# Kernel optimization log

Measured on AMD Instinct MI355X. Metric: run time of the kernel, lower is better.

Reference implementation:

```python
import jax, jax.numpy as jnp
import numpy as np

H = 1024   # d_model
N = 64     # state size (N//2 complex modes)
L_VAL = 4096
DT_MIN, DT_MAX = 1e-3, 0.1


def setup_inputs() -> dict:
    key = jax.random.key(0)
    k1, k2 = jax.random.split(key, 2)
    log_dt = (jax.random.uniform(k1, (H,), dtype=jnp.float32)
              * (np.float32(np.log(DT_MAX)) - np.float32(np.log(DT_MIN)))
              + np.float32(np.log(DT_MIN)))
    C_real = jax.random.normal(k2, (H, N // 2, 2), dtype=jnp.float32)
    # parameterization='exp': log_A_real = log(0.5)
    log_A_real = jnp.full((H, N // 2), np.float32(np.log(0.5)), dtype=jnp.float32)
    A_imag = np.float32(np.pi) * jnp.broadcast_to(
        jnp.arange(N // 2, dtype=jnp.float32), (H, N // 2))
    return {"C_real": C_real, "log_dt": log_dt, "log_A_real": log_A_real,
            "A_imag": A_imag, "L": L_VAL}


def reference(C_real, log_dt, log_A_real, A_imag, L):
    dt = jnp.exp(log_dt)                              # (H,)
    C = C_real[..., 0] + 1j * C_real[..., 1]          # (H, N/2) complex
    A = -jnp.exp(log_A_real) + 1j * A_imag            # (H, N/2) complex ('exp' param)
    dtA = A * dt[:, None]                             # (H, N/2)
    # C <- C * (exp(dtA) - 1) / A
    Ct = C * (jnp.exp(dtA) - 1.0) / A                 # (H, N/2)
    # Vandermonde: exp(dtA[:, :, None] * arange(L)) -> (H, N/2, L)
    V = jnp.exp(dtA[:, :, None] * jnp.arange(L, dtype=jnp.float32))
    K = 2.0 * jnp.einsum('hn,hnl->hl', Ct, V).real    # (H, L) real
    return K
```

## Files before the change

### kernel.cpp

```cpp
#include <hip/hip_runtime.h>
#include <math.h>

#define NMODES 32
#define INV2PI 0.15915494309189535f

typedef short bf16x8 __attribute__((ext_vector_type(8)));
typedef float f32x4  __attribute__((ext_vector_type(4)));

__device__ inline void sincos_rev(float rev, float& s, float& c) {
    float f = rev - floorf(rev);
    s = __builtin_amdgcn_sinf(f);
    c = __builtin_amdgcn_cosf(f);
}

__device__ inline void split_bf(float x, short& hi, short& lo) {
    const unsigned u = __float_as_uint(x);
    const float xf = __uint_as_float(u & 0xFFFF0000u);
    hi = (short)(u >> 16);
    const float r = x - xf;
    lo = (short)(__float_as_uint(r) >> 16);
}

__global__ __launch_bounds__(256, 4) void ssm_mfma_kernel(
    const float* __restrict__ C_real,
    const float* __restrict__ log_dt,
    const float* __restrict__ log_A_real,
    const float* __restrict__ A_imag,
    float* __restrict__ K,
    int L)
{
    __shared__ bf16x8 ldsB[16][64];

    const int h    = blockIdx.x;
    const int tid  = threadIdx.x;
    const int w    = tid >> 6;
    const int lane = tid & 63;
    const int r    = lane & 15;
    const int g    = lane >> 4;

    const float dt = __expf(log_dt[h]);

    float dAr_[8], rhi_[8], rlo_[8], Ctr_[8], Cti_[8];

#pragma unroll
    for (int j = 0; j < 8; ++j) {
        const int m   = g * 8 + j;
        const int idx = h * NMODES + m;
        const float Ar = -__expf(log_A_real[idx]);
        const float Ai = A_imag[idx];
        const float dAr = dt * Ar;
        const float dAi_rev = dt * Ai * INV2PI;

        const float rhi = __uint_as_float(__float_as_uint(dAi_rev) & 0xFFFFF000u);
        const float rlo = dAi_rev - rhi;

        float sn, cs;
        sincos_rev(dAi_rev, sn, cs);
        const float er   = __expf(dAr);
        const float em1r = er * cs - 1.0f;
        const float em1i = er * sn;
        const float inv  = 1.0f / (Ar * Ar + Ai * Ai);
        const float fr   = (em1r * Ar + em1i * Ai) * inv;
        const float fi   = (em1i * Ar - em1r * Ai) * inv;
        const float Cr   = C_real[idx * 2 + 0];
        const float Ci   = C_real[idx * 2 + 1];
        Ctr_[j] = Cr * fr - Ci * fi;
        Cti_[j] = Cr * fi + Ci * fr;
        dAr_[j] = dAr; rhi_[j] = rhi; rlo_[j] = rlo;
    }

    {
        bf16x8 bh0, bl0, bh1, bl1;
        const float d = (float)(r + 16 * w);
#pragma unroll
        for (int j = 0; j < 8; ++j) {
            const float pm = __expf(dAr_[j] * d);
            const float p  = rhi_[j] * d;
            const float f  = (p - floorf(p)) + rlo_[j] * d;
            float qs, qc;
            sincos_rev(f, qs, qc);
            short hh, ll;
            split_bf(pm * qc, hh, ll); bh0[j] = hh; bl0[j] = ll;
            split_bf(pm * qs, hh, ll); bh1[j] = hh; bl1[j] = ll;
        }
        ldsB[w * 4 + 0][lane] = bh0;
        ldsB[w * 4 + 1][lane] = bl0;
        ldsB[w * 4 + 2][lane] = bh1;
        ldsB[w * 4 + 3][lane] = bl1;
    }

    bf16x8 Ah0, Al0, Ah1, Al1;
    {
        const float t = (float)(64 * (r + 16 * w));
#pragma unroll
        for (int j = 0; j < 8; ++j) {
            const float pm = __expf(dAr_[j] * t);
            const float p  = rhi_[j] * t;
            const float f  = (p - floorf(p)) + rlo_[j] * t;
            float zs, zc;
            sincos_rev(f, zs, zc);
            const float gr  = (Ctr_[j] * zc - Cti_[j] * zs) * pm;
            const float gni = -(Ctr_[j] * zs + Cti_[j] * zc) * pm;
            short hh, ll;
            split_bf(gr, hh, ll);  Ah0[j] = hh; Al0[j] = ll;
            split_bf(gni, hh, ll); Ah1[j] = hh; Al1[j] = ll;
        }
    }

    __syncthreads();

    float* __restrict__ Kh = K + (size_t)h * L;

#pragma unroll
    for (int b = 0; b < 4; ++b) {
        const bf16x8 Bh0 = ldsB[b * 4 + 0][lane];
        const bf16x8 Bl0 = ldsB[b * 4 + 1][lane];
        const bf16x8 Bh1 = ldsB[b * 4 + 2][lane];
        const bf16x8 Bl1 = ldsB[b * 4 + 3][lane];
        f32x4 acc = {0.f, 0.f, 0.f, 0.f};
        acc = __builtin_amdgcn_mfma_f32_16x16x32_bf16(Ah0, Bh0, acc, 0, 0, 0);
        acc = __builtin_amdgcn_mfma_f32_16x16x32_bf16(Ah1, Bh1, acc, 0, 0, 0);
        acc = __builtin_amdgcn_mfma_f32_16x16x32_bf16(Ah0, Bl0, acc, 0, 0, 0);
        acc = __builtin_amdgcn_mfma_f32_16x16x32_bf16(Ah1, Bl1, acc, 0, 0, 0);
        acc = __builtin_amdgcn_mfma_f32_16x16x32_bf16(Al0, Bh0, acc, 0, 0, 0);
        acc = __builtin_amdgcn_mfma_f32_16x16x32_bf16(Al1, Bh1, acc, 0, 0, 0);
#pragma unroll
        for (int reg = 0; reg < 4; ++reg) {
            Kh[64 * (16 * w + 4 * g + reg) + 16 * b + r] = 2.0f * acc[reg];
        }
    }
}

extern "C" void kernel_launch(void* const* d_in, const int* in_sizes, int n_in,
                              void* d_out, int out_size, void* d_ws, size_t ws_size,
                              hipStream_t stream) {
    const float* C_real     = (const float*)d_in[0];
    const float* log_dt     = (const float*)d_in[1];
    const float* log_A_real = (const float*)d_in[2];
    const float* A_imag     = (const float*)d_in[3];
    float* K = (float*)d_out;

    const int H = in_sizes[1];
    const int L = out_size / H;

    ssm_mfma_kernel<<<H, 256, 0, stream>>>(
        C_real, log_dt, log_A_real, A_imag, K, L);
}
```

Before: 14.16 us.

## Compute per-mode coefficients once via LDS and swap MFMA operands for float4 stores

```diff
diff --git a/kernel.cpp b/kernel.cpp
--- a/kernel.cpp
+++ b/kernel.cpp
@@ -29,7 +29,9 @@
     float* __restrict__ K,
     int L)
 {
-    __shared__ bf16x8 ldsB[16][64];
+    __shared__ __align__(16) float sDAr[NMODES], sRhi[NMODES], sRlo[NMODES],
+                                   sCtr[NMODES], sCti[NMODES];
+    __shared__ bf16x8 sB[16][64];
 
     const int h    = blockIdx.x;
     const int tid  = threadIdx.x;
@@ -38,14 +40,10 @@
     const int r    = lane & 15;
     const int g    = lane >> 4;
 
-    const float dt = __expf(log_dt[h]);
-
-    float dAr_[8], rhi_[8], rlo_[8], Ctr_[8], Cti_[8];
-
-#pragma unroll
-    for (int j = 0; j < 8; ++j) {
-        const int m   = g * 8 + j;
+    {
+        const int m   = tid & 31;
         const int idx = h * NMODES + m;
+        const float dt = __expf(log_dt[h]);
         const float Ar = -__expf(log_A_real[idx]);
         const float Ai = A_imag[idx];
         const float dAr = dt * Ar;
@@ -64,9 +62,40 @@
         const float fi   = (em1i * Ar - em1r * Ai) * inv;
         const float Cr   = C_real[idx * 2 + 0];
         const float Ci   = C_real[idx * 2 + 1];
-        Ctr_[j] = Cr * fr - Ci * fi;
-        Cti_[j] = Cr * fi + Ci * fr;
-        dAr_[j] = dAr; rhi_[j] = rhi; rlo_[j] = rlo;
+        if (tid < 32) {
+            sDAr[m] = dAr; sRhi[m] = rhi; sRlo[m] = rlo;
+            sCtr[m] = Cr * fr - Ci * fi;
+            sCti[m] = Cr * fi + Ci * fr;
+        }
+    }
+    __syncthreads();
+
+    float dAr_[8], rhi_[8], rlo_[8];
+#pragma unroll
+    for (int j = 0; j < 8; ++j) {
+        dAr_[j] = sDAr[g * 8 + j];
+        rhi_[j] = sRhi[g * 8 + j];
+        rlo_[j] = sRlo[g * 8 + j];
+    }
+
+    bf16x8 Ah0, Al0, Ah1, Al1;
+    {
+        const float t = (float)(64 * (r + 16 * w));
+#pragma unroll
+        for (int j = 0; j < 8; ++j) {
+            const float Ctr = sCtr[g * 8 + j];
+            const float Cti = sCti[g * 8 + j];
+            const float pm = __expf(dAr_[j] * t);
+            const float p  = rhi_[j] * t;
+            const float f  = (p - floorf(p)) + rlo_[j] * t;
+            float zs, zc;
+            sincos_rev(f, zs, zc);
+            const float gr  = (Ctr * zc - Cti * zs) * pm;
+            const float gni = -(Ctr * zs + Cti * zc) * pm;
+            short hh, ll;
+            split_bf(gr, hh, ll);  Ah0[j] = hh; Al0[j] = ll;
+            split_bf(gni, hh, ll); Ah1[j] = hh; Al1[j] = ll;
+        }
     }
 
     {
@@ -83,51 +112,32 @@
             split_bf(pm * qc, hh, ll); bh0[j] = hh; bl0[j] = ll;
             split_bf(pm * qs, hh, ll); bh1[j] = hh; bl1[j] = ll;
         }
-        ldsB[w * 4 + 0][lane] = bh0;
-        ldsB[w * 4 + 1][lane] = bl0;
-        ldsB[w * 4 + 2][lane] = bh1;
-        ldsB[w * 4 + 3][lane] = bl1;
+        sB[w * 4 + 0][lane] = bh0;
+        sB[w * 4 + 1][lane] = bl0;
+        sB[w * 4 + 2][lane] = bh1;
+        sB[w * 4 + 3][lane] = bl1;
     }
-
-    bf16x8 Ah0, Al0, Ah1, Al1;
-    {
-        const float t = (float)(64 * (r + 16 * w));
-#pragma unroll
-        for (int j = 0; j < 8; ++j) {
-            const float pm = __expf(dAr_[j] * t);
-            const float p  = rhi_[j] * t;
-            const float f  = (p - floorf(p)) + rlo_[j] * t;
-            float zs, zc;
-            sincos_rev(f, zs, zc);
-            const float gr  = (Ctr_[j] * zc - Cti_[j] * zs) * pm;
-            const float gni = -(Ctr_[j] * zs + Cti_[j] * zc) * pm;
-            short hh, ll;
-            split_bf(gr, hh, ll);  Ah0[j] = hh; Al0[j] = ll;
-            split_bf(gni, hh, ll); Ah1[j] = hh; Al1[j] = ll;
-        }
-    }
-
     __syncthreads();
 
-    float* __restrict__ Kh = K + (size_t)h * L;
+    float* __restrict__ base = K + (size_t)h * L + 64 * (16 * w + r) + 4 * g;
 
 #pragma unroll
     for (int b = 0; b < 4; ++b) {
-        const bf16x8 Bh0 = ldsB[b * 4 + 0][lane];
-        const bf16x8 Bl0 = ldsB[b * 4 + 1][lane];
-        const bf16x8 Bh1 = ldsB[b * 4 + 2][lane];
-        const bf16x8 Bl1 = ldsB[b * 4 + 3][lane];
+        const bf16x8 Qh0 = sB[b * 4 + 0][lane];
+        const bf16x8 Ql0 = sB[b * 4 + 1][lane];
+        const bf16x8 Qh1 = sB[b * 4 + 2][lane];
+        const bf16x8 Ql1 = sB[b * 4 + 3][lane];
         f32x4 acc = {0.f, 0.f, 0.f, 0.f};
-        acc = __builtin_amdgcn_mfma_f32_16x16x32_bf16(Ah0, Bh0, acc, 0, 0, 0);
-        acc = __builtin_amdgcn_mfma_f32_16x16x32_bf16(Ah1, Bh1, acc, 0, 0, 0);
-        acc = __builtin_amdgcn_mfma_f32_16x16x32_bf16(Ah0, Bl0, acc, 0, 0, 0);
-        acc = __builtin_amdgcn_mfma_f32_16x16x32_bf16(Ah1, Bl1, acc, 0, 0, 0);
-        acc = __builtin_amdgcn_mfma_f32_16x16x32_bf16(Al0, Bh0, acc, 0, 0, 0);
-        acc = __builtin_amdgcn_mfma_f32_16x16x32_bf16(Al1, Bh1, acc, 0, 0, 0);
-#pragma unroll
-        for (int reg = 0; reg < 4; ++reg) {
-            Kh[64 * (16 * w + 4 * g + reg) + 16 * b + r] = 2.0f * acc[reg];
-        }
+        acc = __builtin_amdgcn_mfma_f32_16x16x32_bf16(Qh0, Ah0, acc, 0, 0, 0);
+        acc = __builtin_amdgcn_mfma_f32_16x16x32_bf16(Qh1, Ah1, acc, 0, 0, 0);
+        acc = __builtin_amdgcn_mfma_f32_16x16x32_bf16(Ql0, Ah0, acc, 0, 0, 0);
+        acc = __builtin_amdgcn_mfma_f32_16x16x32_bf16(Ql1, Ah1, acc, 0, 0, 0);
+        acc = __builtin_amdgcn_mfma_f32_16x16x32_bf16(Qh0, Al0, acc, 0, 0, 0);
+        acc = __builtin_amdgcn_mfma_f32_16x16x32_bf16(Qh1, Al1, acc, 0, 0, 0);
+        float4 o;
+        o.x = 2.0f * acc[0]; o.y = 2.0f * acc[1];
+        o.z = 2.0f * acc[2]; o.w = 2.0f * acc[3];
+        *(float4*)(base + 16 * b) = o;
     }
 }
 
```

New measurement: 12.27 us. -13.3%, faster.
